# Kernel optimization log

Hardware: AMD Instinct MI355X
Metric: run time of the kernel (lower is better)

Reference implementation:

```python
import jax, jax.numpy as jnp
import numpy as np

H = 128   # local_channels (hidden_size)
I = 128   # global_channels (input_size)
T = 30    # future_steps
M = 6     # num_modes
N = 8192  # num agents
MIN_SCALE = 0.001
LN_EPS = 1e-5


def layernorm(x, g, b):
    mu = jnp.mean(x, axis=-1, keepdims=True)
    var = jnp.var(x, axis=-1, keepdims=True)
    return (x - mu) * jax.lax.rsqrt(var + LN_EPS) * g + b


def setup_inputs() -> dict:
    key = jax.random.key(0)
    ks = jax.random.split(key, 24)

    def rn(k, shape, s=0.02):
        return jax.random.normal(k, shape, dtype=jnp.float32) * s

    return {
        "local_embed": jax.random.normal(ks[0], (N, H), jnp.float32),
        "global_embed": jax.random.normal(ks[1], (M, N, I), jnp.float32),
        # GRU params (PyTorch layout: gates ordered r, z, n)
        "W_ih": rn(ks[2], (3 * H, I)), "W_hh": rn(ks[3], (3 * H, H)),
        "b_ih": jnp.zeros((3 * H,), jnp.float32), "b_hh": jnp.zeros((3 * H,), jnp.float32),
        # loc head: Linear(H,H) -> LN -> ReLU -> Linear(H,2)
        "loc1_w": rn(ks[4], (H, H)), "loc1_b": jnp.zeros((H,), jnp.float32),
        "loc_ln_g": jnp.ones((H,), jnp.float32), "loc_ln_b": jnp.zeros((H,), jnp.float32),
        "loc2_w": rn(ks[5], (2, H)), "loc2_b": jnp.zeros((2,), jnp.float32),
        # scale head: same structure
        "sc1_w": rn(ks[6], (H, H)), "sc1_b": jnp.zeros((H,), jnp.float32),
        "sc_ln_g": jnp.ones((H,), jnp.float32), "sc_ln_b": jnp.zeros((H,), jnp.float32),
        "sc2_w": rn(ks[7], (2, H)), "sc2_b": jnp.zeros((2,), jnp.float32),
        # pi head: Linear(H+I,H)->LN->ReLU->Linear(H,H)->LN->ReLU->Linear(H,1)
        "pi1_w": rn(ks[8], (H, H + I)), "pi1_b": jnp.zeros((H,), jnp.float32),
        "pi_ln1_g": jnp.ones((H,), jnp.float32), "pi_ln1_b": jnp.zeros((H,), jnp.float32),
        "pi2_w": rn(ks[9], (H, H)), "pi2_b": jnp.zeros((H,), jnp.float32),
        "pi_ln2_g": jnp.ones((H,), jnp.float32), "pi_ln2_b": jnp.zeros((H,), jnp.float32),
        "pi3_w": rn(ks[10], (1, H)), "pi3_b": jnp.zeros((1,), jnp.float32),
    }


def reference(local_embed, global_embed, W_ih, W_hh, b_ih, b_hh,
              loc1_w, loc1_b, loc_ln_g, loc_ln_b, loc2_w, loc2_b,
              sc1_w, sc1_b, sc_ln_g, sc_ln_b, sc2_w, sc2_b,
              pi1_w, pi1_b, pi_ln1_g, pi_ln1_b, pi2_w, pi2_b,
              pi_ln2_g, pi_ln2_b, pi3_w, pi3_b):
    # pi head: cat(broadcast local [M,N,H], global [M,N,I]) -> MLP -> [N, M]
    pi_in = jnp.concatenate(
        (jnp.broadcast_to(local_embed, (M, N, H)), global_embed), axis=-1)
    h1 = jax.nn.relu(layernorm(pi_in @ pi1_w.T + pi1_b, pi_ln1_g, pi_ln1_b))
    h2 = jax.nn.relu(layernorm(h1 @ pi2_w.T + pi2_b, pi_ln2_g, pi_ln2_b))
    pi = (h2 @ pi3_w.T + pi3_b)[..., 0].T  # [N, M]

    # GRU: input is the SAME x at every timestep -> precompute input gates once
    x = global_embed.reshape(M * N, I)                  # [B, I], B = M*N
    gx = x @ W_ih.T + b_ih                              # [B, 3H]
    xr, xz, xn = jnp.split(gx, 3, axis=-1)
    h0 = jnp.tile(local_embed, (M, 1))                  # [B, H]

    def step(h, _):
        gh = h @ W_hh.T + b_hh
        hr, hz, hn = jnp.split(gh, 3, axis=-1)
        r = jax.nn.sigmoid(xr + hr)
        z = jax.nn.sigmoid(xz + hz)
        n = jnp.tanh(xn + r * hn)
        h_new = (1.0 - z) * n + z * h
        return h_new, h_new

    _, outs = jax.lax.scan(step, h0, None, length=T)    # [T, B, H]
    out = jnp.transpose(outs, (1, 0, 2))                # [B, T, H]

    loc = jax.nn.relu(layernorm(out @ loc1_w.T + loc1_b, loc_ln_g, loc_ln_b)) @ loc2_w.T + loc2_b
    sc = jax.nn.relu(layernorm(out @ sc1_w.T + sc1_b, sc_ln_g, sc_ln_b)) @ sc2_w.T + sc2_b
    scale = jax.nn.elu(sc) + 1.0 + MIN_SCALE

    traj = jnp.concatenate((loc, scale), axis=-1).reshape(M, N, T, 4)
    return traj, pi
```

## Files before the change

### kernel.cpp

```cpp
#include <hip/hip_runtime.h>
#include <math.h>

#define H 128
#define I_DIM 128
#define T_STEPS 30
#define M_MODES 6
#define N_AG 8192
#define B_TOT (M_MODES * N_AG)
#define LN_EPS 1e-5f
#define MIN_SCALE 0.001f
#define LOG2E 1.44269504088896f

typedef short bf16x8 __attribute__((ext_vector_type(8)));
typedef float f32x4 __attribute__((ext_vector_type(4)));

#define MFMA16x16x32(A, B, C) __builtin_amdgcn_mfma_f32_16x16x32_bf16(A, B, C, 0, 0, 0)

__device__ __forceinline__ unsigned cvt_pk(float lo, float hi) {
    unsigned r;
    asm("v_cvt_pk_bf16_f32 %0, %1, %2" : "=v"(r) : "v"(lo), "v"(hi));
    return r;
}

__device__ __forceinline__ uint4 pack8(float4 a, float4 b) {
    uint4 r;
    r.x = cvt_pk(a.x, a.y); r.y = cvt_pk(a.z, a.w);
    r.z = cvt_pk(b.x, b.y); r.w = cvt_pk(b.z, b.w);
    return r;
}

__device__ __forceinline__ bf16x8 load8_cvt(const float* __restrict__ p) {
    return __builtin_bit_cast(bf16x8, pack8(((const float4*)p)[0], ((const float4*)p)[1]));
}

__device__ __forceinline__ bf16x8 load8_cvt_s(const float* __restrict__ p, float s) {
    float4 a = ((const float4*)p)[0];
    float4 b = ((const float4*)p)[1];
    a.x*=s; a.y*=s; a.z*=s; a.w*=s;
    b.x*=s; b.y*=s; b.z*=s; b.w*=s;
    return __builtin_bit_cast(bf16x8, pack8(a, b));
}

__device__ __forceinline__ short f2b(float f) {
    union { float f; unsigned u; } v; v.f = f;
    return (short)((v.u + 0x7FFFu + ((v.u >> 16) & 1u)) >> 16);
}

__device__ __forceinline__ float tanh2(float yp) {
    return 1.f - 2.f * __builtin_amdgcn_rcpf(1.f + __builtin_amdgcn_exp2f(yp));
}

__device__ __forceinline__ float elu1(float v) {
    return v > 0.f ? (v + (1.0f + MIN_SCALE))
                   : (__builtin_amdgcn_exp2f(v * LOG2E) + MIN_SCALE);
}

#define DPP_ADD(v, ctrl)                                                     \
    v += __builtin_bit_cast(float, __builtin_amdgcn_mov_dpp(                 \
             __builtin_bit_cast(int, v), ctrl, 0xF, 0xF, true))

__device__ __forceinline__ float red16(float v) {
    DPP_ADD(v, 0xB1);
    DPP_ADD(v, 0x4E);
    DPP_ADD(v, 0x124);
    DPP_ADD(v, 0x128);
    return v;
}

#define HB0 0
#define HB1 8704
#define PI_INBF_OFF   0
#define PI_H1_OFF     33792
#define PI_REDL_OFF   51200
#define PI_RED3_OFF   53248
#define SM_BYTES      54272

__global__ __launch_bounds__(512, 2) void fused_kernel(
    const float* __restrict__ local_embed, const float* __restrict__ global_embed,
    const float* __restrict__ W_ih, const float* __restrict__ W_hh,
    const float* __restrict__ b_ih, const float* __restrict__ b_hh,
    int ntiles, int F,
    const float* __restrict__ loc1_w, const float* __restrict__ loc1_b,
    const float* __restrict__ loc_ln_g, const float* __restrict__ loc_ln_b,
    const float* __restrict__ loc2_w, const float* __restrict__ loc2_b,
    const float* __restrict__ sc1_w, const float* __restrict__ sc1_b,
    const float* __restrict__ sc_ln_g, const float* __restrict__ sc_ln_b,
    const float* __restrict__ sc2_w, const float* __restrict__ sc2_b,
    float* __restrict__ traj,
    const float* __restrict__ pi1_w, const float* __restrict__ pi1_b,
    const float* __restrict__ ln1_g, const float* __restrict__ ln1_b,
    const float* __restrict__ pi2_w, const float* __restrict__ pi2_b,
    const float* __restrict__ ln2_g, const float* __restrict__ ln2_b,
    const float* __restrict__ pi3_w, const float* __restrict__ pi3_b,
    float* __restrict__ pi_out)
{
    __shared__ __align__(16) char smraw[SM_BYTES];

    const int tid = threadIdx.x;
    const int w  = tid >> 6;
    const int l  = tid & 63;
    const int ln = l & 15;
    const int lg = l >> 4;

    if (w < 4) {
        float bias_ih[3][2], bhn[2];
        #pragma unroll
        for (int u = 0; u < 2; ++u) {
            const int c = 32*w + 16*u + ln;
            bhn[u] = b_hh[2*H + c] * (2.f * LOG2E);
            #pragma unroll
            for (int g = 0; g < 3; ++g) {
                const float sc = (g < 2) ? LOG2E : (2.f * LOG2E);
                bias_ih[g][u] = (b_ih[g*H + c] + (g < 2 ? b_hh[g*H + c] : 0.f)) * sc;
            }
        }
        const int ro = ln*272 + lg*16;
        const int wb = (lg*4)*272 + (32*w + ln)*2;
        const int sr_ = tid >> 3;
        const int ssg = tid & 7;

        bf16x8 wf[3][2][4];

        for (int it = blockIdx.x; it < ntiles; it += F) {
            const int lb0 = it * 32;
            __syncthreads();

            {
                const int n = (lb0 + sr_) & (N_AG - 1);
                const float* src = local_embed + (size_t)n * H;
                #pragma unroll
                for (int hseg = 0; hseg < 2; ++hseg) {
                    const int s8 = ssg + hseg*8;
                    const float4 a = ((const float4*)(src + s8*8))[0];
                    const float4 c = ((const float4*)(src + s8*8))[1];
                    *(uint4*)(smraw + HB0 + sr_*272 + s8*16) = pack8(a, c);
                }
            }

            float h_reg[2][2][4];
            #pragma unroll
            for (int grp = 0; grp < 2; ++grp)
                #pragma unroll
                for (int u = 0; u < 2; ++u) {
                    const int j = 32*w + 16*u + ln;
                    #pragma unroll
                    for (int rg = 0; rg < 4; ++rg) {
                        const int n = (lb0 + grp*16 + lg*4 + rg) & (N_AG - 1);
                        h_reg[grp][u][rg] = local_embed[(size_t)n * H + j];
                    }
                }

            #pragma unroll
            for (int u = 0; u < 2; ++u)
                #pragma unroll
                for (int g = 0; g < 3; ++g) {
                    const int crow = g*H + 32*w + 16*u + ln;
                    const float sc = (g < 2) ? LOG2E : (2.f * LOG2E);
                    #pragma unroll
                    for (int kt = 0; kt < 4; ++kt)
                        wf[g][u][kt] = load8_cvt_s(W_ih + (size_t)crow * I_DIM + kt*32 + lg*8, sc);
                }
            __syncthreads();

            float gx[2][3][2][4];
            #pragma unroll
            for (int grp = 0; grp < 2; ++grp) {
                bf16x8 ax[4];
                #pragma unroll
                for (int kt = 0; kt < 4; ++kt)
                    ax[kt] = *(const bf16x8*)(smraw + HB1 + ro + grp*4352 + kt*64);
                f32x4 ag[3][2];
                #pragma unroll
                for (int g = 0; g < 3; ++g)
                    #pragma unroll
                    for (int u = 0; u < 2; ++u) ag[g][u] = (f32x4)(0.f);
                __builtin_amdgcn_s_setprio(1);
                #pragma unroll
                for (int kt = 0; kt < 4; ++kt)
                    #pragma unroll
                    for (int g = 0; g < 3; ++g)
                        #pragma unroll
                        for (int u = 0; u < 2; ++u)
                            ag[g][u] = MFMA16x16x32(ax[kt], wf[g][u][kt], ag[g][u]);
                __builtin_amdgcn_s_setprio(0);
                #pragma unroll
                for (int g = 0; g < 3; ++g)
                    #pragma unroll
                    for (int u = 0; u < 2; ++u)
                        #pragma unroll
                        for (int rg = 0; rg < 4; ++rg)
                            gx[grp][g][u][rg] = ag[g][u][rg] + bias_ih[g][u];
            }

            #pragma unroll
            for (int u = 0; u < 2; ++u)
                #pragma unroll
                for (int g = 0; g < 3; ++g) {
                    const int crow = g*H + 32*w + 16*u + ln;
                    const float sc = (g < 2) ? LOG2E : (2.f * LOG2E);
                    #pragma unroll
                    for (int kt = 0; kt < 4; ++kt)
                        wf[g][u][kt] = load8_cvt_s(W_hh + (size_t)crow * H + kt*32 + lg*8, sc);
                }
            __syncthreads();

            int rd_off = HB0, wr_off = HB1;
            for (int i = 0; i <= T_STEPS; ++i) {
                if (i < T_STEPS) {
                    #pragma unroll
                    for (int grp = 0; grp < 2; ++grp) {
                        bf16x8 af[4];
                        #pragma unroll
                        for (int kt = 0; kt < 4; ++kt)
                            af[kt] = *(const bf16x8*)(smraw + rd_off + ro + grp*4352 + kt*64);

                        f32x4 ga[3][2];
                        #pragma unroll
                        for (int g = 0; g < 3; ++g)
                            #pragma unroll
                            for (int u = 0; u < 2; ++u) ga[g][u] = (f32x4)(0.f);
                        __builtin_amdgcn_s_setprio(1);
                        #pragma unroll
                        for (int kt = 0; kt < 4; ++kt)
                            #pragma unroll
                            for (int g = 0; g < 3; ++g)
                                #pragma unroll
                                for (int u = 0; u < 2; ++u)
                                    ga[g][u] = MFMA16x16x32(af[kt], wf[g][u][kt], ga[g][u]);
                        __builtin_amdgcn_s_setprio(0);

                        #pragma unroll
                        for (int u = 0; u < 2; ++u) {
                            float hv[4];
                            #pragma unroll
                            for (int rg = 0; rg < 4; ++rg) {
                                const float ea = __builtin_amdgcn_exp2f(-(gx[grp][0][u][rg] + ga[0][u][rg]));
                                const float eb = __builtin_amdgcn_exp2f(-(gx[grp][1][u][rg] + ga[1][u][rg]));
                                const float A = 1.f + ea;
                                const float Bv_ = 1.f + eb;
                                const float R = __builtin_amdgcn_rcpf(A * Bv_);
                                const float rr = R * Bv_;
                                const float zz = R * A;
                                const float nn = tanh2(gx[grp][2][u][rg] + rr * (ga[2][u][rg] + bhn[u]));
                                const float h  = nn + zz * (h_reg[grp][u][rg] - nn);
                                h_reg[grp][u][rg] = h;
                                hv[rg] = h;
                            }
                            const unsigned p0 = cvt_pk(hv[0], hv[1]);
                            const unsigned p1 = cvt_pk(hv[2], hv[3]);
                            const int wa = wr_off + wb + grp*4352 + u*32;
                            *(short*)(smraw + wa)        = (short)p0;
                            *(short*)(smraw + wa + 272)  = (short)(p0 >> 16);
                            *(short*)(smraw + wa + 544)  = (short)p1;
                            *(short*)(smraw + wa + 816)  = (short)(p1 >> 16);
                        }
                    }
                }
                __syncthreads();
                rd_off ^= 8704; wr_off ^= 8704;
            }
        }
    } else {
        const int hw = w - 4;
        const int hd = hw & 1;
        const int mrow = (hw >> 1) * 16;

        const float* __restrict__ W1  = hd ? sc1_w   : loc1_w;
        const float* __restrict__ B1v = hd ? sc1_b   : loc1_b;
        const float* __restrict__ Gv  = hd ? sc_ln_g : loc_ln_g;
        const float* __restrict__ Bv  = hd ? sc_ln_b : loc_ln_b;
        const float* __restrict__ W2  = hd ? sc2_w   : loc2_w;
        const float* __restrict__ B2v = hd ? sc2_b   : loc2_b;

        bf16x8 whf[8][4];
        float bias1[8], lng[8], lnb[8], w2a[8], w2b[8];
        #pragma unroll
        for (int nt = 0; nt < 8; ++nt) {
            const int c = 16*nt + ln;
            #pragma unroll
            for (int kt = 0; kt < 4; ++kt)
                whf[nt][kt] = load8_cvt(W1 + (size_t)c * H + kt*32 + lg*8);
            bias1[nt] = B1v[c]; lng[nt] = Gv[c]; lnb[nt] = Bv[c];
            w2a[nt] = W2[c];    w2b[nt] = W2[H + c];
        }
        const float b2_0 = B2v[0], b2_1 = B2v[1];
        const int ho = (mrow + ln)*272 + lg*16;
        const int sr_ = (tid - 256) >> 3;
        const int ssg = tid & 7;

        for (int it = blockIdx.x; it < ntiles; it += F) {
            const int lb0 = it * 32;
            __syncthreads();

            {
                const float* src = global_embed + (size_t)(lb0 + sr_) * I_DIM;
                #pragma unroll
                for (int hseg = 0; hseg < 2; ++hseg) {
                    const int s8 = ssg + hseg*8;
                    const float4 a = ((const float4*)(src + s8*8))[0];
                    const float4 c = ((const float4*)(src + s8*8))[1];
                    *(uint4*)(smraw + HB1 + sr_*272 + s8*16) = pack8(a, c);
                }
            }
            __syncthreads();
            __syncthreads();

            int rd_off = HB0;
            float2 pend[4];
            for (int i = 0; i <= T_STEPS; ++i) {
                if (i >= 2 && ln == 0) {
                    #pragma unroll
                    for (int rg = 0; rg < 4; ++rg) {
                        const int b = lb0 + mrow + lg*4 + rg;
                        *(float2*)(traj + ((size_t)b * T_STEPS + (i - 2)) * 4 + hd*2) = pend[rg];
                    }
                }
                if (i >= 1) {
                    bf16x8 af[4];
                    #pragma unroll
                    for (int kt = 0; kt < 4; ++kt)
                        af[kt] = *(const bf16x8*)(smraw + rd_off + ho + kt*64);

                    f32x4 acc[8];
                    #pragma unroll
                    for (int nt = 0; nt < 8; ++nt) acc[nt] = (f32x4)(0.f);
                    __builtin_amdgcn_s_setprio(1);
                    #pragma unroll
                    for (int kt = 0; kt < 4; ++kt)
                        #pragma unroll
                        for (int nt = 0; nt < 8; ++nt)
                            acc[nt] = MFMA16x16x32(af[kt], whf[nt][kt], acc[nt]);
                    __builtin_amdgcn_s_setprio(0);

                    #pragma unroll
                    for (int rg = 0; rg < 4; ++rg) {
                        float s = 0.f, q = 0.f;
                        #pragma unroll
                        for (int nt = 0; nt < 8; ++nt) {
                            const float a = acc[nt][rg] + bias1[nt];
                            acc[nt][rg] = a;
                            s += a; q += a*a;
                        }
                        s = red16(s);
                        q = red16(q);
                        const float mu = s * (1.f/H);
                        const float var = q * (1.f/H) - mu*mu;
                        const float rs = rsqrtf(var + LN_EPS);
                        const float murs = mu * rs;
                        float p0 = 0.f, p1 = 0.f;
                        #pragma unroll
                        for (int nt = 0; nt < 8; ++nt) {
                            float v = fmaf(fmaf(acc[nt][rg], rs, -murs), lng[nt], lnb[nt]);
                            v = fmaxf(v, 0.f);
                            p0 = fmaf(v, w2a[nt], p0);
                            p1 = fmaf(v, w2b[nt], p1);
                        }
                        p0 = red16(p0);
                        p1 = red16(p1);
                        float v0 = p0 + b2_0;
                        float v1 = p1 + b2_1;
                        if (hd) {
                            v0 = elu1(v0);
                            v1 = elu1(v1);
                        }
                        pend[rg] = make_float2(v0, v1);
                    }
                }
                __syncthreads();
                rd_off ^= 8704;
            }
            if (ln == 0) {
                #pragma unroll
                for (int rg = 0; rg < 4; ++rg) {
                    const int b = lb0 + mrow + lg*4 + rg;
                    *(float2*)(traj + ((size_t)b * T_STEPS + (T_STEPS - 1)) * 4 + hd*2) = pend[rg];
                }
            }
        }
    }

    {
        const int sub  = tid >> 8;
        const int stid = tid & 255;
        const int w4 = stid >> 6;

        short (*inbf)[264] = (short(*)[264])(smraw + PI_INBF_OFF + (size_t)sub*16896);
        short (*h1bf)[136] = (short(*)[136])(smraw + PI_H1_OFF   + (size_t)sub*8704);
        float (*redL)[32][2] = (float(*)[32][2])(smraw + PI_REDL_OFF + (size_t)sub*1024);
        float (*red3)[32]    = (float(*)[32])(smraw + PI_RED3_OFF + (size_t)sub*512);

        bf16x8 wf1[2][8];
        bf16x8 wf2[2][4];
        float b1[2], g1[2], bb1[2], b2[2], g2[2], bb2[2], w3[2];
        #pragma unroll
        for (int nt = 0; nt < 2; ++nt) {
            const int c = 32*w4 + 16*nt + ln;
            #pragma unroll
            for (int kt = 0; kt < 8; ++kt)
                wf1[nt][kt] = load8_cvt(pi1_w + (size_t)c * (2*H) + kt*32 + lg*8);
            #pragma unroll
            for (int kt = 0; kt < 4; ++kt)
                wf2[nt][kt] = load8_cvt(pi2_w + (size_t)c * H + kt*32 + lg*8);
            b1[nt] = pi1_b[c]; g1[nt] = ln1_g[c]; bb1[nt] = ln1_b[c];
            b2[nt] = pi2_b[c]; g2[nt] = ln2_g[c]; bb2[nt] = ln2_b[c];
            w3[nt] = pi3_w[c];
        }
        const float b3 = pi3_b[0];

        const int r0 = ((int)blockIdx.x*2 + sub) * 32;
        __syncthreads();
        {
            const int r   = stid >> 3;
            const int seg = stid & 7;
            const int b = r0 + r;
            const int n = b & (N_AG - 1);
            const float* src = (seg < 4) ? (local_embed + (size_t)n * H + seg * 32)
                                         : (global_embed + (size_t)b * I_DIM + (seg - 4) * 32);
            #pragma unroll
            for (int i = 0; i < 4; ++i) {
                const float4 a = ((const float4*)src)[2*i];
                const float4 c = ((const float4*)src)[2*i+1];
                *(uint4*)&inbf[r][seg*32 + i*8] = pack8(a, c);
            }
        }
        __syncthreads();

        f32x4 acc1[2][2];
        #pragma unroll
        for (int m = 0; m < 2; ++m) {
            #pragma unroll
            for (int nt = 0; nt < 2; ++nt) acc1[m][nt] = (f32x4)(0.f);
            bf16x8 af[8];
            #pragma unroll
            for (int kt = 0; kt < 8; ++kt)
                af[kt] = *(const bf16x8*)&inbf[m*16 + ln][kt*32 + lg*8];
            __builtin_amdgcn_s_setprio(1);
            #pragma unroll
            for (int kt = 0; kt < 8; ++kt)
                #pragma unroll
                for (int nt = 0; nt < 2; ++nt)
                    acc1[m][nt] = MFMA16x16x32(af[kt], wf1[nt][kt], acc1[m][nt]);
            __builtin_amdgcn_s_setprio(0);
        }

        #pragma unroll
        for (int m = 0; m < 2; ++m)
            #pragma unroll
            for (int rg = 0; rg < 4; ++rg) {
                float s = 0.f, q = 0.f;
                #pragma unroll
                for (int nt = 0; nt < 2; ++nt) {
                    const float a = acc1[m][nt][rg] + b1[nt];
                    acc1[m][nt][rg] = a;
                    s += a; q += a*a;
                }
                s = red16(s);
                q = red16(q);
                if (ln == 0) {
                    const int row = m*16 + lg*4 + rg;
                    redL[w4][row][0] = s;
                    redL[w4][row][1] = q;
                }
            }
        __syncthreads();

        #pragma unroll
        for (int m = 0; m < 2; ++m)
            #pragma unroll
            for (int rg = 0; rg < 4; ++rg) {
                const int row = m*16 + lg*4 + rg;
                const float S = redL[0][row][0] + redL[1][row][0] + redL[2][row][0] + redL[3][row][0];
                const float Q = redL[0][row][1] + redL[1][row][1] + redL[2][row][1] + redL[3][row][1];
                const float mu = S * (1.f/H);
                const float var = Q * (1.f/H) - mu*mu;
                const float rs = rsqrtf(var + LN_EPS);
                #pragma unroll
                for (int nt = 0; nt < 2; ++nt) {
                    const float v = fmaxf((acc1[m][nt][rg] - mu) * rs * g1[nt] + bb1[nt], 0.f);
                    h1bf[row][32*w4 + 16*nt + ln] = f2b(v);
                }
            }
        __syncthreads();

        f32x4 acc2[2][2];
        #pragma unroll
        for (int m = 0; m < 2; ++m) {
            #pragma unroll
            for (int nt = 0; nt < 2; ++nt) acc2[m][nt] = (f32x4)(0.f);
            bf16x8 af[4];
            #pragma unroll
            for (int kt = 0; kt < 4; ++kt)
                af[kt] = *(const bf16x8*)&h1bf[m*16 + ln][kt*32 + lg*8];
            __builtin_amdgcn_s_setprio(1);
            #pragma unroll
            for (int kt = 0; kt < 4; ++kt)
                #pragma unroll
                for (int nt = 0; nt < 2; ++nt)
                    acc2[m][nt] = MFMA16x16x32(af[kt], wf2[nt][kt], acc2[m][nt]);
            __builtin_amdgcn_s_setprio(0);
        }

        #pragma unroll
        for (int m = 0; m < 2; ++m)
            #pragma unroll
            for (int rg = 0; rg < 4; ++rg) {
                float s = 0.f, q = 0.f;
                #pragma unroll
                for (int nt = 0; nt < 2; ++nt) {
                    const float a = acc2[m][nt][rg] + b2[nt];
                    acc2[m][nt][rg] = a;
                    s += a; q += a*a;
                }
                s = red16(s);
                q = red16(q);
                if (ln == 0) {
                    const int row = m*16 + lg*4 + rg;
                    redL[w4][row][0] = s;
                    redL[w4][row][1] = q;
                }
            }
        __syncthreads();

        #pragma unroll
        for (int m = 0; m < 2; ++m)
            #pragma unroll
            for (int rg = 0; rg < 4; ++rg) {
                const int row = m*16 + lg*4 + rg;
                const float S = redL[0][row][0] + redL[1][row][0] + redL[2][row][0] + redL[3][row][0];
                const float Q = redL[0][row][1] + redL[1][row][1] + redL[2][row][1] + redL[3][row][1];
                const float mu = S * (1.f/H);
                const float var = Q * (1.f/H) - mu*mu;
                const float rs = rsqrtf(var + LN_EPS);
                float p2 = 0.f;
                #pragma unroll
                for (int nt = 0; nt < 2; ++nt) {
                    const float v = fmaxf((acc2[m][nt][rg] - mu) * rs * g2[nt] + bb2[nt], 0.f);
                    p2 = fmaf(v, w3[nt], p2);
                }
                p2 = red16(p2);
                if (ln == 0) red3[w4][row] = p2;
            }
        __syncthreads();

        if (stid < 32) {
            const int row = stid;
            const float pv = red3[0][row] + red3[1][row] + red3[2][row] + red3[3][row] + b3;
            const int b = r0 + row;
            const int n = b & (N_AG - 1);
            const int m = b >> 13;
            pi_out[(size_t)n * M_MODES + m] = pv;
        }
    }
}

extern "C" void kernel_launch(void* const* d_in, const int* in_sizes, int n_in,
                              void* d_out, int out_size, void* d_ws, size_t ws_size,
                              hipStream_t stream) {
    (void)in_sizes; (void)n_in; (void)out_size; (void)d_ws; (void)ws_size;
    const float* local_embed  = (const float*)d_in[0];
    const float* global_embed = (const float*)d_in[1];
    const float* W_ih   = (const float*)d_in[2];
    const float* W_hh   = (const float*)d_in[3];
    const float* b_ih   = (const float*)d_in[4];
    const float* b_hh   = (const float*)d_in[5];
    const float* loc1_w = (const float*)d_in[6];
    const float* loc1_b = (const float*)d_in[7];
    const float* loc_ln_g = (const float*)d_in[8];
    const float* loc_ln_b = (const float*)d_in[9];
    const float* loc2_w = (const float*)d_in[10];
    const float* loc2_b = (const float*)d_in[11];
    const float* sc1_w  = (const float*)d_in[12];
    const float* sc1_b  = (const float*)d_in[13];
    const float* sc_ln_g = (const float*)d_in[14];
    const float* sc_ln_b = (const float*)d_in[15];
    const float* sc2_w  = (const float*)d_in[16];
    const float* sc2_b  = (const float*)d_in[17];
    const float* pi1_w  = (const float*)d_in[18];
    const float* pi1_b  = (const float*)d_in[19];
    const float* pi_ln1_g = (const float*)d_in[20];
    const float* pi_ln1_b = (const float*)d_in[21];
    const float* pi2_w  = (const float*)d_in[22];
    const float* pi2_b  = (const float*)d_in[23];
    const float* pi_ln2_g = (const float*)d_in[24];
    const float* pi_ln2_b = (const float*)d_in[25];
    const float* pi3_w  = (const float*)d_in[26];
    const float* pi3_b  = (const float*)d_in[27];

    float* traj = (float*)d_out;
    float* pi_out = traj + (size_t)B_TOT * T_STEPS * 4;

    const int ntiles = B_TOT / 32;
    const int F = 768;

    fused_kernel<<<F, 512, 0, stream>>>(
        local_embed, global_embed, W_ih, W_hh, b_ih, b_hh,
        ntiles, F,
        loc1_w, loc1_b, loc_ln_g, loc_ln_b, loc2_w, loc2_b,
        sc1_w, sc1_b, sc_ln_g, sc_ln_b, sc2_w, sc2_b, traj,
        pi1_w, pi1_b, pi_ln1_g, pi_ln1_b,
        pi2_w, pi2_b, pi_ln2_g, pi_ln2_b, pi3_w, pi3_b, pi_out);
}
```

Before: 520.2 us.

## Double tile to 64 rows per block with LDS-spilled input gates, one block per CU

Each block now handles 64 rows instead of 32. The GRU recurrence runs four row groups per warp, keeping the input-gate precompute for two groups in registers and spilling the other two to a new LDS region. The input-gate values are used to initialise the MFMA accumulators, which removes an add per element. Launch bounds drop to one block per CU with a 256-block grid, and the head warps and pi section are extended to match. The aim is to spread each barrier and weight-load cost over more rows, at the price of lower occupancy, more LDS and extra LDS traffic every step.

```diff
diff --git a/kernel.cpp b/kernel.cpp
--- a/kernel.cpp
+++ b/kernel.cpp
@@ -68,14 +68,15 @@
 }
 
 #define HB0 0
-#define HB1 8704
+#define HB1 17408
+#define GX23 34816
 #define PI_INBF_OFF   0
 #define PI_H1_OFF     33792
 #define PI_REDL_OFF   51200
 #define PI_RED3_OFF   53248
-#define SM_BYTES      54272
-
-__global__ __launch_bounds__(512, 2) void fused_kernel(
+#define SM_BYTES      90112
+
+__global__ __launch_bounds__(512, 1) void fused_kernel(
     const float* __restrict__ local_embed, const float* __restrict__ global_embed,
     const float* __restrict__ W_ih, const float* __restrict__ W_hh,
     const float* __restrict__ b_ih, const float* __restrict__ b_hh,
@@ -120,26 +121,30 @@
         const int ssg = tid & 7;
 
         bf16x8 wf[3][2][4];
+        f32x4 gxrz[2][2][2];
+        f32x4 gxn[2][2];
 
         for (int it = blockIdx.x; it < ntiles; it += F) {
-            const int lb0 = it * 32;
-            __syncthreads();
-
-            {
-                const int n = (lb0 + sr_) & (N_AG - 1);
+            const int lb0 = it * 64;
+            __syncthreads();
+
+            #pragma unroll
+            for (int rr2 = 0; rr2 < 2; ++rr2) {
+                const int r = sr_ + rr2*32;
+                const int n = (lb0 + r) & (N_AG - 1);
                 const float* src = local_embed + (size_t)n * H;
                 #pragma unroll
                 for (int hseg = 0; hseg < 2; ++hseg) {
                     const int s8 = ssg + hseg*8;
                     const float4 a = ((const float4*)(src + s8*8))[0];
                     const float4 c = ((const float4*)(src + s8*8))[1];
-                    *(uint4*)(smraw + HB0 + sr_*272 + s8*16) = pack8(a, c);
-                }
-            }
-
-            float h_reg[2][2][4];
-            #pragma unroll
-            for (int grp = 0; grp < 2; ++grp)
+                    *(uint4*)(smraw + HB0 + r*272 + s8*16) = pack8(a, c);
+                }
+            }
+
+            float h_reg[4][2][4];
+            #pragma unroll
+            for (int grp = 0; grp < 4; ++grp)
                 #pragma unroll
                 for (int u = 0; u < 2; ++u) {
                     const int j = 32*w + 16*u + ln;
@@ -162,9 +167,8 @@
                 }
             __syncthreads();
 
-            float gx[2][3][2][4];
-            #pragma unroll
-            for (int grp = 0; grp < 2; ++grp) {
+            #pragma unroll
+            for (int grp = 0; grp < 4; ++grp) {
                 bf16x8 ax[4];
                 #pragma unroll
                 for (int kt = 0; kt < 4; ++kt)
@@ -189,7 +193,24 @@
                     for (int u = 0; u < 2; ++u)
                         #pragma unroll
                         for (int rg = 0; rg < 4; ++rg)
-                            gx[grp][g][u][rg] = ag[g][u][rg] + bias_ih[g][u];
+                            ag[g][u][rg] += bias_ih[g][u];
+                if (grp < 2) {
+                    #pragma unroll
+                    for (int u = 0; u < 2; ++u) {
+                        gxrz[grp][0][u] = ag[0][u];
+                        gxrz[grp][1][u] = ag[1][u];
+                        gxn[grp][u]     = ag[2][u];
+                    }
+                } else {
+                    const int r23 = (grp - 2)*16 + lg*4;
+                    #pragma unroll
+                    for (int g = 0; g < 3; ++g)
+                        #pragma unroll
+                        for (int u = 0; u < 2; ++u) {
+                            const int ch = g*H + 32*w + 16*u + ln;
+                            *(f32x4*)(smraw + GX23 + ((ch*36 + r23) << 2)) = ag[g][u];
+                        }
+                }
             }
 
             #pragma unroll
@@ -208,17 +229,34 @@
             for (int i = 0; i <= T_STEPS; ++i) {
                 if (i < T_STEPS) {
                     #pragma unroll
-                    for (int grp = 0; grp < 2; ++grp) {
+                    for (int grp = 0; grp < 4; ++grp) {
                         bf16x8 af[4];
                         #pragma unroll
                         for (int kt = 0; kt < 4; ++kt)
                             af[kt] = *(const bf16x8*)(smraw + rd_off + ro + grp*4352 + kt*64);
 
                         f32x4 ga[3][2];
-                        #pragma unroll
-                        for (int g = 0; g < 3; ++g)
+                        f32x4 gxn_l[2];
+                        if (grp < 2) {
                             #pragma unroll
-                            for (int u = 0; u < 2; ++u) ga[g][u] = (f32x4)(0.f);
+                            for (int u = 0; u < 2; ++u) {
+                                ga[0][u] = gxrz[grp][0][u];
+                                ga[1][u] = gxrz[grp][1][u];
+                                ga[2][u] = (f32x4)(0.f);
+                                gxn_l[u] = gxn[grp][u];
+                            }
+                        } else {
+                            const int r23 = (grp - 2)*16 + lg*4;
+                            #pragma unroll
+                            for (int u = 0; u < 2; ++u) {
+                                const int ch = 32*w + 16*u + ln;
+                                ga[0][u] = *(const f32x4*)(smraw + GX23 + ((ch*36 + r23) << 2));
+                                ga[1][u] = *(const f32x4*)(smraw + GX23 + (((H + ch)*36 + r23) << 2));
+                                ga[2][u] = (f32x4)(0.f);
+                                gxn_l[u] = *(const f32x4*)(smraw + GX23 + (((2*H + ch)*36 + r23) << 2));
+                            }
+                        }
+
                         __builtin_amdgcn_s_setprio(1);
                         #pragma unroll
                         for (int kt = 0; kt < 4; ++kt)
@@ -234,14 +272,14 @@
                             float hv[4];
                             #pragma unroll
                             for (int rg = 0; rg < 4; ++rg) {
-                                const float ea = __builtin_amdgcn_exp2f(-(gx[grp][0][u][rg] + ga[0][u][rg]));
-                                const float eb = __builtin_amdgcn_exp2f(-(gx[grp][1][u][rg] + ga[1][u][rg]));
-                                const float A = 1.f + ea;
+                                const float ea = __builtin_amdgcn_exp2f(-ga[0][u][rg]);
+                                const float eb = __builtin_amdgcn_exp2f(-ga[1][u][rg]);
+                                const float A  = 1.f + ea;
                                 const float Bv_ = 1.f + eb;
                                 const float R = __builtin_amdgcn_rcpf(A * Bv_);
                                 const float rr = R * Bv_;
                                 const float zz = R * A;
-                                const float nn = tanh2(gx[grp][2][u][rg] + rr * (ga[2][u][rg] + bhn[u]));
+                                const float nn = tanh2(gxn_l[u][rg] + rr * (ga[2][u][rg] + bhn[u]));
                                 const float h  = nn + zz * (h_reg[grp][u][rg] - nn);
                                 h_reg[grp][u][rg] = h;
                                 hv[rg] = h;
@@ -257,13 +295,13 @@
                     }
                 }
                 __syncthreads();
-                rd_off ^= 8704; wr_off ^= 8704;
+                rd_off ^= 17408; wr_off ^= 17408;
             }
         }
     } else {
         const int hw = w - 4;
         const int hd = hw & 1;
-        const int mrow = (hw >> 1) * 16;
+        const int mrow0 = (hw >> 1) * 16;
 
         const float* __restrict__ W1  = hd ? sc1_w   : loc1_w;
         const float* __restrict__ B1v = hd ? sc1_b   : loc1_b;
@@ -284,97 +322,106 @@
             w2a[nt] = W2[c];    w2b[nt] = W2[H + c];
         }
         const float b2_0 = B2v[0], b2_1 = B2v[1];
-        const int ho = (mrow + ln)*272 + lg*16;
         const int sr_ = (tid - 256) >> 3;
         const int ssg = tid & 7;
 
         for (int it = blockIdx.x; it < ntiles; it += F) {
-            const int lb0 = it * 32;
-            __syncthreads();
-
-            {
-                const float* src = global_embed + (size_t)(lb0 + sr_) * I_DIM;
+            const int lb0 = it * 64;
+            __syncthreads();
+
+            #pragma unroll
+            for (int rr2 = 0; rr2 < 2; ++rr2) {
+                const int r = sr_ + rr2*32;
+                const float* src = global_embed + (size_t)(lb0 + r) * I_DIM;
                 #pragma unroll
                 for (int hseg = 0; hseg < 2; ++hseg) {
                     const int s8 = ssg + hseg*8;
                     const float4 a = ((const float4*)(src + s8*8))[0];
                     const float4 c = ((const float4*)(src + s8*8))[1];
-                    *(uint4*)(smraw + HB1 + sr_*272 + s8*16) = pack8(a, c);
+                    *(uint4*)(smraw + HB1 + r*272 + s8*16) = pack8(a, c);
                 }
             }
             __syncthreads();
             __syncthreads();
 
             int rd_off = HB0;
-            float2 pend[4];
+            float2 pend[2][4];
             for (int i = 0; i <= T_STEPS; ++i) {
                 if (i >= 2 && ln == 0) {
                     #pragma unroll
+                    for (int rr = 0; rr < 2; ++rr)
+                        #pragma unroll
+                        for (int rg = 0; rg < 4; ++rg) {
+                            const int b = lb0 + mrow0 + rr*32 + lg*4 + rg;
+                            *(float2*)(traj + ((size_t)b * T_STEPS + (i - 2)) * 4 + hd*2) = pend[rr][rg];
+                        }
+                }
+                if (i >= 1) {
+                    #pragma unroll
+                    for (int rr = 0; rr < 2; ++rr) {
+                        const int ho = (mrow0 + rr*32 + ln)*272 + lg*16;
+                        bf16x8 af[4];
+                        #pragma unroll
+                        for (int kt = 0; kt < 4; ++kt)
+                            af[kt] = *(const bf16x8*)(smraw + rd_off + ho + kt*64);
+
+                        f32x4 acc[8];
+                        #pragma unroll
+                        for (int nt = 0; nt < 8; ++nt) acc[nt] = (f32x4)(0.f);
+                        __builtin_amdgcn_s_setprio(1);
+                        #pragma unroll
+                        for (int kt = 0; kt < 4; ++kt)
+                            #pragma unroll
+                            for (int nt = 0; nt < 8; ++nt)
+                                acc[nt] = MFMA16x16x32(af[kt], whf[nt][kt], acc[nt]);
+                        __builtin_amdgcn_s_setprio(0);
+
+                        #pragma unroll
+                        for (int rg = 0; rg < 4; ++rg) {
+                            float s = 0.f, q = 0.f;
+                            #pragma unroll
+                            for (int nt = 0; nt < 8; ++nt) {
+                                const float a = acc[nt][rg] + bias1[nt];
+                                acc[nt][rg] = a;
+                                s += a; q += a*a;
+                            }
+                            s = red16(s);
+                            q = red16(q);
+                            const float mu = s * (1.f/H);
+                            const float var = q * (1.f/H) - mu*mu;
+                            const float rs = rsqrtf(var + LN_EPS);
+                            const float murs = mu * rs;
+                            float p0 = 0.f, p1 = 0.f;
+                            #pragma unroll
+                            for (int nt = 0; nt < 8; ++nt) {
+                                float v = fmaf(fmaf(acc[nt][rg], rs, -murs), lng[nt], lnb[nt]);
+                                v = fmaxf(v, 0.f);
+                                p0 = fmaf(v, w2a[nt], p0);
+                                p1 = fmaf(v, w2b[nt], p1);
+                            }
+                            p0 = red16(p0);
+                            p1 = red16(p1);
+                            float v0 = p0 + b2_0;
+                            float v1 = p1 + b2_1;
+                            if (hd) {
+                                v0 = elu1(v0);
+                                v1 = elu1(v1);
+                            }
+                            pend[rr][rg] = make_float2(v0, v1);
+                        }
+                    }
+                }
+                __syncthreads();
+                rd_off ^= 17408;
+            }
+            if (ln == 0) {
+                #pragma unroll
+                for (int rr = 0; rr < 2; ++rr)
+                    #pragma unroll
                     for (int rg = 0; rg < 4; ++rg) {
-                        const int b = lb0 + mrow + lg*4 + rg;
-                        *(float2*)(traj + ((size_t)b * T_STEPS + (i - 2)) * 4 + hd*2) = pend[rg];
-                    }
-                }
-                if (i >= 1) {
-                    bf16x8 af[4];
-                    #pragma unroll
-                    for (int kt = 0; kt < 4; ++kt)
-                        af[kt] = *(const bf16x8*)(smraw + rd_off + ho + kt*64);
-
-                    f32x4 acc[8];
-                    #pragma unroll
-                    for (int nt = 0; nt < 8; ++nt) acc[nt] = (f32x4)(0.f);
-                    __builtin_amdgcn_s_setprio(1);
-                    #pragma unroll
-                    for (int kt = 0; kt < 4; ++kt)
-                        #pragma unroll
-                        for (int nt = 0; nt < 8; ++nt)
-                            acc[nt] = MFMA16x16x32(af[kt], whf[nt][kt], acc[nt]);
-                    __builtin_amdgcn_s_setprio(0);
-
-                    #pragma unroll
-                    for (int rg = 0; rg < 4; ++rg) {
-                        float s = 0.f, q = 0.f;
-                        #pragma unroll
-                        for (int nt = 0; nt < 8; ++nt) {
-                            const float a = acc[nt][rg] + bias1[nt];
-                            acc[nt][rg] = a;
-                            s += a; q += a*a;
-                        }
-                        s = red16(s);
-                        q = red16(q);
-                        const float mu = s * (1.f/H);
-                        const float var = q * (1.f/H) - mu*mu;
-                        const float rs = rsqrtf(var + LN_EPS);
-                        const float murs = mu * rs;
-                        float p0 = 0.f, p1 = 0.f;
-                        #pragma unroll
-                        for (int nt = 0; nt < 8; ++nt) {
-                            float v = fmaf(fmaf(acc[nt][rg], rs, -murs), lng[nt], lnb[nt]);
-                            v = fmaxf(v, 0.f);
-                            p0 = fmaf(v, w2a[nt], p0);
-                            p1 = fmaf(v, w2b[nt], p1);
-                        }
-                        p0 = red16(p0);
-                        p1 = red16(p1);
-                        float v0 = p0 + b2_0;
-                        float v1 = p1 + b2_1;
-                        if (hd) {
-                            v0 = elu1(v0);
-                            v1 = elu1(v1);
-                        }
-                        pend[rg] = make_float2(v0, v1);
-                    }
-                }
-                __syncthreads();
-                rd_off ^= 8704;
-            }
-            if (ln == 0) {
-                #pragma unroll
-                for (int rg = 0; rg < 4; ++rg) {
-                    const int b = lb0 + mrow + lg*4 + rg;
-                    *(float2*)(traj + ((size_t)b * T_STEPS + (T_STEPS - 1)) * 4 + hd*2) = pend[rg];
-                }
+                        const int b = lb0 + mrow0 + rr*32 + lg*4 + rg;
+                        *(float2*)(traj + ((size_t)b * T_STEPS + (T_STEPS - 1)) * 4 + hd*2) = pend[rr][rg];
+                    }
             }
         }
     }
@@ -407,148 +454,150 @@
         }
         const float b3 = pi3_b[0];
 
-        const int r0 = ((int)blockIdx.x*2 + sub) * 32;
-        __syncthreads();
-        {
-            const int r   = stid >> 3;
-            const int seg = stid & 7;
-            const int b = r0 + r;
-            const int n = b & (N_AG - 1);
-            const float* src = (seg < 4) ? (local_embed + (size_t)n * H + seg * 32)
-                                         : (global_embed + (size_t)b * I_DIM + (seg - 4) * 32);
-            #pragma unroll
-            for (int i = 0; i < 4; ++i) {
-                const float4 a = ((const float4*)src)[2*i];
-                const float4 c = ((const float4*)src)[2*i+1];
-                *(uint4*)&inbf[r][seg*32 + i*8] = pack8(a, c);
-            }
-        }
-        __syncthreads();
-
-        f32x4 acc1[2][2];
-        #pragma unroll
-        for (int m = 0; m < 2; ++m) {
-            #pragma unroll
-            for (int nt = 0; nt < 2; ++nt) acc1[m][nt] = (f32x4)(0.f);
-            bf16x8 af[8];
-            #pragma unroll
-            for (int kt = 0; kt < 8; ++kt)
-                af[kt] = *(const bf16x8*)&inbf[m*16 + ln][kt*32 + lg*8];
-            __builtin_amdgcn_s_setprio(1);
-            #pragma unroll
-            for (int kt = 0; kt < 8; ++kt)
-                #pragma unroll
-                for (int nt = 0; nt < 2; ++nt)
-                    acc1[m][nt] = MFMA16x16x32(af[kt], wf1[nt][kt], acc1[m][nt]);
-            __builtin_amdgcn_s_setprio(0);
-        }
-
-        #pragma unroll
-        for (int m = 0; m < 2; ++m)
-            #pragma unroll
-            for (int rg = 0; rg < 4; ++rg) {
-                float s = 0.f, q = 0.f;
-                #pragma unroll
-                for (int nt = 0; nt < 2; ++nt) {
-                    const float a = acc1[m][nt][rg] + b1[nt];
-                    acc1[m][nt][rg] = a;
-                    s += a; q += a*a;
-                }
-                s = red16(s);
-                q = red16(q);
-                if (ln == 0) {
+        for (int p = 0; p < 3; ++p) {
+            const int r0 = (((int)blockIdx.x*3 + p)*2 + sub) * 32;
+            __syncthreads();
+            {
+                const int r   = stid >> 3;
+                const int seg = stid & 7;
+                const int b = r0 + r;
+                const int n = b & (N_AG - 1);
+                const float* src = (seg < 4) ? (local_embed + (size_t)n * H + seg * 32)
+                                             : (global_embed + (size_t)b * I_DIM + (seg - 4) * 32);
+                #pragma unroll
+                for (int i = 0; i < 4; ++i) {
+                    const float4 a = ((const float4*)src)[2*i];
+                    const float4 c = ((const float4*)src)[2*i+1];
+                    *(uint4*)&inbf[r][seg*32 + i*8] = pack8(a, c);
+                }
+            }
+            __syncthreads();
+
+            f32x4 acc1[2][2];
+            #pragma unroll
+            for (int m = 0; m < 2; ++m) {
+                #pragma unroll
+                for (int nt = 0; nt < 2; ++nt) acc1[m][nt] = (f32x4)(0.f);
+                bf16x8 af[8];
+                #pragma unroll
+                for (int kt = 0; kt < 8; ++kt)
+                    af[kt] = *(const bf16x8*)&inbf[m*16 + ln][kt*32 + lg*8];
+                __builtin_amdgcn_s_setprio(1);
+                #pragma unroll
+                for (int kt = 0; kt < 8; ++kt)
+                    #pragma unroll
+                    for (int nt = 0; nt < 2; ++nt)
+                        acc1[m][nt] = MFMA16x16x32(af[kt], wf1[nt][kt], acc1[m][nt]);
+                __builtin_amdgcn_s_setprio(0);
+            }
+
+            #pragma unroll
+            for (int m = 0; m < 2; ++m)
+                #pragma unroll
+                for (int rg = 0; rg < 4; ++rg) {
+                    float s = 0.f, q = 0.f;
+                    #pragma unroll
+                    for (int nt = 0; nt < 2; ++nt) {
+                        const float a = acc1[m][nt][rg] + b1[nt];
+                        acc1[m][nt][rg] = a;
+                        s += a; q += a*a;
+                    }
+                    s = red16(s);
+                    q = red16(q);
+                    if (ln == 0) {
+                        const int row = m*16 + lg*4 + rg;
+                        redL[w4][row][0] = s;
+                        redL[w4][row][1] = q;
+                    }
+                }
+            __syncthreads();
+
+            #pragma unroll
+            for (int m = 0; m < 2; ++m)
+                #pragma unroll
+                for (int rg = 0; rg < 4; ++rg) {
                     const int row = m*16 + lg*4 + rg;
-                    redL[w4][row][0] = s;
-                    redL[w4][row][1] = q;
-                }
-            }
-        __syncthreads();
-
-        #pragma unroll
-        for (int m = 0; m < 2; ++m)
-            #pragma unroll
-            for (int rg = 0; rg < 4; ++rg) {
-                const int row = m*16 + lg*4 + rg;
-                const float S = redL[0][row][0] + redL[1][row][0] + redL[2][row][0] + redL[3][row][0];
-                const float Q = redL[0][row][1] + redL[1][row][1] + redL[2][row][1] + redL[3][row][1];
-                const float mu = S * (1.f/H);
-                const float var = Q * (1.f/H) - mu*mu;
-                const float rs = rsqrtf(var + LN_EPS);
-                #pragma unroll
-                for (int nt = 0; nt < 2; ++nt) {
-                    const float v = fmaxf((acc1[m][nt][rg] - mu) * rs * g1[nt] + bb1[nt], 0.f);
-                    h1bf[row][32*w4 + 16*nt + ln] = f2b(v);
-                }
-            }
-        __syncthreads();
-
-        f32x4 acc2[2][2];
-        #pragma unroll
-        for (int m = 0; m < 2; ++m) {
-            #pragma unroll
-            for (int nt = 0; nt < 2; ++nt) acc2[m][nt] = (f32x4)(0.f);
-            bf16x8 af[4];
-            #pragma unroll
-            for (int kt = 0; kt < 4; ++kt)
-                af[kt] = *(const bf16x8*)&h1bf[m*16 + ln][kt*32 + lg*8];
-            __builtin_amdgcn_s_setprio(1);
-            #pragma unroll
-            for (int kt = 0; kt < 4; ++kt)
-                #pragma unroll
-                for (int nt = 0; nt < 2; ++nt)
-                    acc2[m][nt] = MFMA16x16x32(af[kt], wf2[nt][kt], acc2[m][nt]);
-            __builtin_amdgcn_s_setprio(0);
-        }
-
-        #pragma unroll
-        for (int m = 0; m < 2; ++m)
-            #pragma unroll
-            for (int rg = 0; rg < 4; ++rg) {
-                float s = 0.f, q = 0.f;
-                #pragma unroll
-                for (int nt = 0; nt < 2; ++nt) {
-                    const float a = acc2[m][nt][rg] + b2[nt];
-                    acc2[m][nt][rg] = a;
-                    s += a; q += a*a;
-                }
-                s = red16(s);
-                q = red16(q);
-                if (ln == 0) {
+                    const float S = redL[0][row][0] + redL[1][row][0] + redL[2][row][0] + redL[3][row][0];
+                    const float Q = redL[0][row][1] + redL[1][row][1] + redL[2][row][1] + redL[3][row][1];
+                    const float mu = S * (1.f/H);
+                    const float var = Q * (1.f/H) - mu*mu;
+                    const float rs = rsqrtf(var + LN_EPS);
+                    #pragma unroll
+                    for (int nt = 0; nt < 2; ++nt) {
+                        const float v = fmaxf((acc1[m][nt][rg] - mu) * rs * g1[nt] + bb1[nt], 0.f);
+                        h1bf[row][32*w4 + 16*nt + ln] = f2b(v);
+                    }
+                }
+            __syncthreads();
+
+            f32x4 acc2[2][2];
+            #pragma unroll
+            for (int m = 0; m < 2; ++m) {
+                #pragma unroll
+                for (int nt = 0; nt < 2; ++nt) acc2[m][nt] = (f32x4)(0.f);
+                bf16x8 af[4];
+                #pragma unroll
+                for (int kt = 0; kt < 4; ++kt)
+                    af[kt] = *(const bf16x8*)&h1bf[m*16 + ln][kt*32 + lg*8];
+                __builtin_amdgcn_s_setprio(1);
+                #pragma unroll
+                for (int kt = 0; kt < 4; ++kt)
+                    #pragma unroll
+                    for (int nt = 0; nt < 2; ++nt)
+                        acc2[m][nt] = MFMA16x16x32(af[kt], wf2[nt][kt], acc2[m][nt]);
+                __builtin_amdgcn_s_setprio(0);
+            }
+
+            #pragma unroll
+            for (int m = 0; m < 2; ++m)
+                #pragma unroll
+                for (int rg = 0; rg < 4; ++rg) {
+                    float s = 0.f, q = 0.f;
+                    #pragma unroll
+                    for (int nt = 0; nt < 2; ++nt) {
+                        const float a = acc2[m][nt][rg] + b2[nt];
+                        acc2[m][nt][rg] = a;
+                        s += a; q += a*a;
+                    }
+                    s = red16(s);
+                    q = red16(q);
+                    if (ln == 0) {
+                        const int row = m*16 + lg*4 + rg;
+                        redL[w4][row][0] = s;
+                        redL[w4][row][1] = q;
+                    }
+                }
+            __syncthreads();
+
+            #pragma unroll
+            for (int m = 0; m < 2; ++m)
+                #pragma unroll
+                for (int rg = 0; rg < 4; ++rg) {
                     const int row = m*16 + lg*4 + rg;
-                    redL[w4][row][0] = s;
-                    redL[w4][row][1] = q;
-                }
-            }
-        __syncthreads();
-
-        #pragma unroll
-        for (int m = 0; m < 2; ++m)
-            #pragma unroll
-            for (int rg = 0; rg < 4; ++rg) {
-                const int row = m*16 + lg*4 + rg;
-                const float S = redL[0][row][0] + redL[1][row][0] + redL[2][row][0] + redL[3][row][0];
-                const float Q = redL[0][row][1] + redL[1][row][1] + redL[2][row][1] + redL[3][row][1];
-                const float mu = S * (1.f/H);
-                const float var = Q * (1.f/H) - mu*mu;
-                const float rs = rsqrtf(var + LN_EPS);
-                float p2 = 0.f;
-                #pragma unroll
-                for (int nt = 0; nt < 2; ++nt) {
-                    const float v = fmaxf((acc2[m][nt][rg] - mu) * rs * g2[nt] + bb2[nt], 0.f);
-                    p2 = fmaf(v, w3[nt], p2);
-                }
-                p2 = red16(p2);
-                if (ln == 0) red3[w4][row] = p2;
-            }
-        __syncthreads();
-
-        if (stid < 32) {
-            const int row = stid;
-            const float pv = red3[0][row] + red3[1][row] + red3[2][row] + red3[3][row] + b3;
-            const int b = r0 + row;
-            const int n = b & (N_AG - 1);
-            const int m = b >> 13;
-            pi_out[(size_t)n * M_MODES + m] = pv;
+                    const float S = redL[0][row][0] + redL[1][row][0] + redL[2][row][0] + redL[3][row][0];
+                    const float Q = redL[0][row][1] + redL[1][row][1] + redL[2][row][1] + redL[3][row][1];
+                    const float mu = S * (1.f/H);
+                    const float var = Q * (1.f/H) - mu*mu;
+                    const float rs = rsqrtf(var + LN_EPS);
+                    float p2 = 0.f;
+                    #pragma unroll
+                    for (int nt = 0; nt < 2; ++nt) {
+                        const float v = fmaxf((acc2[m][nt][rg] - mu) * rs * g2[nt] + bb2[nt], 0.f);
+                        p2 = fmaf(v, w3[nt], p2);
+                    }
+                    p2 = red16(p2);
+                    if (ln == 0) red3[w4][row] = p2;
+                }
+            __syncthreads();
+
+            if (stid < 32) {
+                const int row = stid;
+                const float pv = red3[0][row] + red3[1][row] + red3[2][row] + red3[3][row] + b3;
+                const int b = r0 + row;
+                const int n = b & (N_AG - 1);
+                const int m = b >> 13;
+                pi_out[(size_t)n * M_MODES + m] = pv;
+            }
         }
     }
 }
@@ -589,8 +638,8 @@
     float* traj = (float*)d_out;
     float* pi_out = traj + (size_t)B_TOT * T_STEPS * 4;
 
-    const int ntiles = B_TOT / 32;
-    const int F = 768;
+    const int ntiles = B_TOT / 64;
+    const int F = 256;
 
     fused_kernel<<<F, 512, 0, stream>>>(
         local_embed, global_embed, W_ih, W_hh, b_ih, b_hh,
```

Result: faster. 486.4 us, median of 2 (-6.5%).
